# Performance work log

Measured on AMD Instinct MI355X. Metric: run time of the kernel, lower is better.

## Reference

```python
import jax, jax.numpy as jnp
import numpy as np

B, S = 1, 2048            # one prefill sequence, flattened to n_tokens = B*S
HID = 4096
NH, NKV, HD = 32, 8, 128  # query heads, kv heads, head dim
G, M = NKV, NH // NKV     # kv groups, query heads per group
THETA = 1e6


def setup_inputs() -> dict:
    key = jax.random.key(0)
    ks = jax.random.split(key, 5)
    h = jax.random.normal(ks[0], (B * S, HID), dtype=jnp.float32)
    position_ids = jnp.tile(jnp.arange(S, dtype=jnp.int32), B)
    wq = jax.random.normal(ks[1], (NH * HD, HID), dtype=jnp.float32) * 0.02
    wk = jax.random.normal(ks[2], (NKV * HD, HID), dtype=jnp.float32) * 0.02
    wv = jax.random.normal(ks[3], (NKV * HD, HID), dtype=jnp.float32) * 0.02
    wo = jax.random.normal(ks[4], (HID, NH * HD), dtype=jnp.float32) * 0.02
    return {"h": h, "position_ids": position_ids, "wq": wq, "wk": wk, "wv": wv, "wo": wo}


def _rope_cos_sin(position_ids):
    # non-interleaved (half-split) RoPE, default inv_freq with theta=1e6
    inv_freq = 1.0 / (THETA ** (jnp.arange(0, HD, 2, dtype=jnp.float32) / HD))  # [HD/2]
    freqs = position_ids.astype(jnp.float32)[:, None] * inv_freq[None, :]       # [n, HD/2]
    return jnp.cos(freqs)[:, None, :], jnp.sin(freqs)[:, None, :]               # broadcast over heads


def _apply_rope(x, cos, sin):
    x1, x2 = jnp.split(x, 2, axis=-1)
    return jnp.concatenate([x1 * cos - x2 * sin, x2 * cos + x1 * sin], axis=-1)


def reference(h, position_ids, wq, wk, wv, wo):
    n = h.shape[0]
    q = (h @ wq.T).reshape(n, NH, HD)
    k = (h @ wk.T).reshape(n, NKV, HD)
    v = (h @ wv.T).reshape(B, S, NKV, HD)

    cos, sin = _rope_cos_sin(position_ids)
    q = _apply_rope(q, cos, sin).reshape(B, S, G, M, HD)
    k = _apply_rope(k, cos, sin).reshape(B, S, G, HD)

    scale = 1.0 / np.sqrt(HD).astype(np.float32)
    # grouped-query attention: each kv head g serves M query heads
    scores = jnp.einsum('bqgmd,bkgd->bgmqk', q, k) * scale      # [B,G,M,S,S]
    causal = jnp.tril(jnp.ones((S, S), dtype=bool))
    scores = jnp.where(causal, scores, jnp.finfo(scores.dtype).min)
    p = jax.nn.softmax(scores, axis=-1)
    o = jnp.einsum('bgmqk,bkgd->bqgmd', p, v).reshape(n, NH * HD)
    return o @ wo.T
```

## Files before the change

kernel.cpp:

```cpp
#include <hip/hip_runtime.h>
#include <hip/hip_bf16.h>

#define S_LEN 2048
#define HID 4096
#define NH 32
#define NKV 8
#define HD 128
#define NQKV 6144

typedef unsigned short u16;
typedef unsigned int u32;
typedef __bf16 bf16x8 __attribute__((ext_vector_type(8)));
typedef float f32x4 __attribute__((ext_vector_type(4)));

__device__ __forceinline__ float bf2f(u16 u) {
    union { u32 i; float f; } x; x.i = ((u32)u) << 16; return x.f;
}
__device__ __forceinline__ u16 f2bf(float f) {
    union { float f; u32 i; } x; x.f = f;
    u32 r = x.i + 0x7fffu + ((x.i >> 16) & 1u);
    return (u16)(r >> 16);
}
__device__ __forceinline__ u32 pack2(float a, float b) {
    return (u32)f2bf(a) | ((u32)f2bf(b) << 16);
}
__device__ __forceinline__ void gld16(const u16* g, u16* l) {
    __builtin_amdgcn_global_load_lds(
        (const __attribute__((address_space(1))) u32*)g,
        (__attribute__((address_space(3))) u32*)l, 16, 0, 0);
}

__global__ __launch_bounds__(256) void cvt_f32_bf16(
    const float* __restrict__ src, u16* __restrict__ dst, int n8)
{
    int i = blockIdx.x * 256 + threadIdx.x;
    if (i >= n8) return;
    const float4* s = (const float4*)src + (size_t)i * 2;
    float4 x0 = s[0], x1 = s[1];
    uint4 p;
    p.x = pack2(x0.x, x0.y); p.y = pack2(x0.z, x0.w);
    p.z = pack2(x1.x, x1.y); p.w = pack2(x1.z, x1.w);
    *((uint4*)dst + i) = p;
}

template <bool OUTBF16>
__global__ __launch_bounds__(256) void gemm128(
    const u16* __restrict__ X, const u16* __restrict__ W,
    void* __restrict__ C, int K, int ldc)
{
    __shared__ __align__(16) u16 As[128 * 32];
    __shared__ __align__(16) u16 Bs[128 * 32];

    const int tid  = threadIdx.x;
    const int w    = tid >> 6;
    const int lane = tid & 63;
    const int quad = lane >> 4;
    const int n16  = lane & 15;

    int id = blockIdx.y * gridDim.x + blockIdx.x;
    const int nwg = gridDim.x * gridDim.y;
    if ((nwg & 7) == 0) {
        const int cpx = nwg >> 3;
        id = (id & 7) * cpx + (id >> 3);
    }
    const int m0 = (id / gridDim.x) * 128;
    const int n0 = (id % gridDim.x) * 128;

    const int wr   = (w >> 1) * 64;
    const int wc   = (w & 1) * 64;

    const int c0 = tid;
    const int c1 = tid + 256;

    f32x4 acc[4][4] = {};

    for (int k0 = 0; k0 < K; k0 += 32) {
        __syncthreads();
        gld16(X + (size_t)(m0 + (c0 >> 2)) * K + k0 + (c0 & 3) * 8,
              As + (size_t)(w * 64) * 8);
        gld16(X + (size_t)(m0 + (c1 >> 2)) * K + k0 + (c1 & 3) * 8,
              As + (size_t)(256 + w * 64) * 8);
        gld16(W + (size_t)(n0 + (c0 >> 2)) * K + k0 + (c0 & 3) * 8,
              Bs + (size_t)(w * 64) * 8);
        gld16(W + (size_t)(n0 + (c1 >> 2)) * K + k0 + (c1 & 3) * 8,
              Bs + (size_t)(256 + w * 64) * 8);
        __syncthreads();

        bf16x8 a[4], b[4];
#pragma unroll
        for (int t = 0; t < 4; ++t) {
            a[t] = *reinterpret_cast<const bf16x8*>(As + (wr + t * 16 + n16) * 32 + quad * 8);
            b[t] = *reinterpret_cast<const bf16x8*>(Bs + (wc + t * 16 + n16) * 32 + quad * 8);
        }
#pragma unroll
        for (int mt = 0; mt < 4; ++mt)
#pragma unroll
            for (int nt = 0; nt < 4; ++nt)
                acc[mt][nt] = __builtin_amdgcn_mfma_f32_16x16x32_bf16(
                    a[mt], b[nt], acc[mt][nt], 0, 0, 0);
    }

#pragma unroll
    for (int mt = 0; mt < 4; ++mt) {
        const int row0 = m0 + wr + mt * 16 + quad * 4;
#pragma unroll
        for (int nt = 0; nt < 4; ++nt) {
            const int col = n0 + wc + nt * 16 + n16;
#pragma unroll
            for (int r = 0; r < 4; ++r) {
                if constexpr (OUTBF16)
                    ((u16*)C)[(size_t)(row0 + r) * ldc + col] = f2bf(acc[mt][nt][r]);
                else
                    ((float*)C)[(size_t)(row0 + r) * ldc + col] = acc[mt][nt][r];
            }
        }
    }
}

template <bool XF32, bool OUTBF16>
__global__ __launch_bounds__(256) void gemm_bt(
    const void* __restrict__ Xv,
    const float* __restrict__ W0, int r1,
    const float* __restrict__ W1, int r2,
    const float* __restrict__ W2,
    void* __restrict__ C, int K, int ldc)
{
    __shared__ u16 Xs[64][48];
    __shared__ u16 Ws[64][48];

    const int tid  = threadIdx.x;
    const int w    = tid >> 6;
    const int lane = tid & 63;
    const int m0   = blockIdx.y * 64;
    const int n0   = blockIdx.x * 64;

    const int sr = tid >> 2;
    const int sc = (tid & 3) * 8;

    const float* xrow32 = nullptr;
    const u16*   xrow16 = nullptr;
    if constexpr (XF32) xrow32 = (const float*)Xv + (size_t)(m0 + sr) * K;
    else                xrow16 = (const u16*)Xv + (size_t)(m0 + sr) * K;

    const int wr = n0 + sr;
    const float* wrow;
    if (wr < r1)      wrow = W0 + (size_t)wr * K;
    else if (wr < r2) wrow = W1 + (size_t)(wr - r1) * K;
    else              wrow = W2 + (size_t)(wr - r2) * K;

    f32x4 acc[4] = {};
    const int mrow = w * 16 + (lane & 15);
    const int nrow = lane & 15;
    const int kq   = (lane >> 4) * 8;

    for (int k0 = 0; k0 < K; k0 += 32) {
        __syncthreads();
        if constexpr (XF32) {
            float4 x0 = *reinterpret_cast<const float4*>(xrow32 + k0 + sc);
            float4 x1 = *reinterpret_cast<const float4*>(xrow32 + k0 + sc + 4);
            uint4 p;
            p.x = pack2(x0.x, x0.y); p.y = pack2(x0.z, x0.w);
            p.z = pack2(x1.x, x1.y); p.w = pack2(x1.z, x1.w);
            *reinterpret_cast<uint4*>(&Xs[sr][sc]) = p;
        } else {
            *reinterpret_cast<uint4*>(&Xs[sr][sc]) =
                *reinterpret_cast<const uint4*>(xrow16 + k0 + sc);
        }
        {
            float4 w0v = *reinterpret_cast<const float4*>(wrow + k0 + sc);
            float4 w1v = *reinterpret_cast<const float4*>(wrow + k0 + sc + 4);
            uint4 p;
            p.x = pack2(w0v.x, w0v.y); p.y = pack2(w0v.z, w0v.w);
            p.z = pack2(w1v.x, w1v.y); p.w = pack2(w1v.z, w1v.w);
            *reinterpret_cast<uint4*>(&Ws[sr][sc]) = p;
        }
        __syncthreads();
        bf16x8 a = *reinterpret_cast<const bf16x8*>(&Xs[mrow][kq]);
#pragma unroll
        for (int t = 0; t < 4; ++t) {
            bf16x8 b = *reinterpret_cast<const bf16x8*>(&Ws[t * 16 + nrow][kq]);
            acc[t] = __builtin_amdgcn_mfma_f32_16x16x32_bf16(a, b, acc[t], 0, 0, 0);
        }
    }

    const int mb = m0 + w * 16 + ((lane >> 4) << 2);
#pragma unroll
    for (int t = 0; t < 4; ++t) {
        const int col = n0 + t * 16 + (lane & 15);
#pragma unroll
        for (int i = 0; i < 4; ++i) {
            if constexpr (OUTBF16)
                ((u16*)C)[(size_t)(mb + i) * ldc + col] = f2bf(acc[t][i]);
            else
                ((float*)C)[(size_t)(mb + i) * ldc + col] = acc[t][i];
        }
    }
}

__global__ __launch_bounds__(256) void rope_kernel(
    const u16* __restrict__ qkv, const int* __restrict__ pos,
    u16* __restrict__ qb, u16* __restrict__ kb, u16* __restrict__ vb)
{
    const int n   = blockIdx.x;
    const int tid = threadIdx.x;
    const float scale = 0.08838834764831845f;
    __shared__ float cs[64], sn[64];
    if (tid < 64) {
        float p   = (float)pos[n];
        float inv = powf(1.0e6f, -(float)tid / 64.0f);
        float f   = p * inv;
        cs[tid] = cosf(f);
        sn[tid] = sinf(f);
    }
    __syncthreads();
    const u16* row = qkv + (size_t)n * NQKV;

    for (int i = tid; i < NH * 64; i += 256) {
        int h = i >> 6, j = i & 63;
        float x1 = bf2f(row[h * HD + j]), x2 = bf2f(row[h * HD + j + 64]);
        size_t base = ((size_t)h * S_LEN + n) * HD;
        qb[base + j]      = f2bf((x1 * cs[j] - x2 * sn[j]) * scale);
        qb[base + j + 64] = f2bf((x2 * cs[j] + x1 * sn[j]) * scale);
    }
    for (int i = tid; i < NKV * 64; i += 256) {
        int g = i >> 6, j = i & 63;
        const u16* kr = row + NH * HD + g * HD;
        float x1 = bf2f(kr[j]), x2 = bf2f(kr[j + 64]);
        size_t base = ((size_t)g * S_LEN + n) * HD;
        kb[base + j]      = f2bf(x1 * cs[j] - x2 * sn[j]);
        kb[base + j + 64] = f2bf(x2 * cs[j] + x1 * sn[j]);
    }
    for (int i = tid; i < NKV * HD; i += 256) {
        int g = i >> 7, d = i & 127;
        vb[((size_t)g * S_LEN + n) * HD + d] = row[NH * HD + NKV * HD + g * HD + d];
    }
}

__global__ __launch_bounds__(256) void attn_mfma(
    const u16* __restrict__ qb, const u16* __restrict__ kb,
    const u16* __restrict__ vb, u16* __restrict__ ao)
{
    __shared__ __align__(16) u16 KPs[64 * 128];
    __shared__ __align__(16) u16 Vt[128 * 64];

    const int tid  = threadIdx.x;
    const int w    = tid >> 6;
    const int lane = tid & 63;
    const int quad = lane >> 4;
    const int n16  = lane & 15;
    const int h    = blockIdx.y;
    const int g    = h >> 2;
    const int NQT  = S_LEN / 64;

    const u16* kbase = kb + (size_t)g * S_LEN * HD;
    const u16* vbase = vb + (size_t)g * S_LEN * HD;
    const int xsw = (n16 & 7) << 3;

    for (int half = 0; half < 2; ++half) {
        const int qt = half ? (NQT - 1 - blockIdx.x) : blockIdx.x;
        const int q0 = qt * 64;

        bf16x8 qf[4];
        {
            const u16* qrow = qb + ((size_t)h * S_LEN + q0 + w * 16 + n16) * HD;
#pragma unroll
            for (int s = 0; s < 4; ++s)
                qf[s] = *reinterpret_cast<const bf16x8*>(qrow + s * 32 + quad * 8);
        }

        f32x4 of[8] = {};
        float mrow[4], lrow[4];
#pragma unroll
        for (int r = 0; r < 4; ++r) { mrow[r] = -1e30f; lrow[r] = 0.0f; }

        uint4 kreg[4], vreg[4];
        auto load_kv = [&](int k0) {
#pragma unroll
            for (int i = 0; i < 4; ++i) {
                kreg[i] = *reinterpret_cast<const uint4*>(
                    kbase + (size_t)(k0 + (tid >> 4) + 16 * i) * HD + (tid & 15) * 8);
                vreg[i] = *reinterpret_cast<const uint4*>(
                    vbase + (size_t)(k0 + lane) * HD + w * 8 + i * 32);
            }
        };
        load_kv(0);

        const int ntiles = qt + 1;
        for (int kt = 0; kt < ntiles; ++kt) {
            __syncthreads();
#pragma unroll
            for (int i = 0; i < 4; ++i) {
                const int key = (tid >> 4) + 16 * i;
                const int d0  = (tid & 15) * 8;
                *reinterpret_cast<uint4*>(
                    &KPs[key * 128 + (d0 ^ ((key & 7) << 3))]) = kreg[i];
            }
#pragma unroll
            for (int i = 0; i < 4; ++i) {
                const int d0 = w * 8 + i * 32;
                const u32 vw[4] = {vreg[i].x, vreg[i].y, vreg[i].z, vreg[i].w};
#pragma unroll
                for (int t = 0; t < 4; ++t) {
                    const int r0 = d0 + 2 * t;
                    Vt[r0 * 64 + (lane ^ ((r0 & 7) << 3))]             = (u16)(vw[t] & 0xffff);
                    Vt[(r0 + 1) * 64 + (lane ^ (((r0 + 1) & 7) << 3))] = (u16)(vw[t] >> 16);
                }
            }
            __syncthreads();
            if (kt + 1 < ntiles) load_kv((kt + 1) * 64);

            f32x4 sc[4] = {};
#pragma unroll
            for (int s = 0; s < 4; ++s) {
#pragma unroll
                for (int t = 0; t < 4; ++t) {
                    bf16x8 bf = *reinterpret_cast<const bf16x8*>(
                        &KPs[(t * 16 + n16) * 128 + ((s * 32 + quad * 8) ^ xsw)]);
                    sc[t] = __builtin_amdgcn_mfma_f32_16x16x32_bf16(qf[s], bf, sc[t], 0, 0, 0);
                }
            }

            if (kt == ntiles - 1) {
                const int qbase = q0 + w * 16 + quad * 4;
#pragma unroll
                for (int t = 0; t < 4; ++t) {
                    int key = kt * 64 + t * 16 + n16;
#pragma unroll
                    for (int r = 0; r < 4; ++r)
                        if (key > qbase + r) sc[t][r] = -1e30f;
                }
            }

            __syncthreads();

#pragma unroll
            for (int r = 0; r < 4; ++r) {
                float mx = fmaxf(fmaxf(sc[0][r], sc[1][r]), fmaxf(sc[2][r], sc[3][r]));
                mx = fmaxf(mx, __shfl_xor(mx, 1));
                mx = fmaxf(mx, __shfl_xor(mx, 2));
                mx = fmaxf(mx, __shfl_xor(mx, 4));
                mx = fmaxf(mx, __shfl_xor(mx, 8));
                float mnew  = fmaxf(mrow[r], mx);
                float alpha = __expf(mrow[r] - mnew);
                float ls = 0.0f;
                const int pr = quad * 4 + r;
#pragma unroll
                for (int t = 0; t < 4; ++t) {
                    float p = __expf(sc[t][r] - mnew);
                    KPs[(w * 16 + pr) * 64 + ((t * 16 + n16) ^ ((pr & 7) << 3))] = f2bf(p);
                    ls += p;
                }
                ls += __shfl_xor(ls, 1);
                ls += __shfl_xor(ls, 2);
                ls += __shfl_xor(ls, 4);
                ls += __shfl_xor(ls, 8);
                lrow[r] = lrow[r] * alpha + ls;
                mrow[r] = mnew;
#pragma unroll
                for (int nt = 0; nt < 8; ++nt) of[nt][r] *= alpha;
            }
            __threadfence_block();

#pragma unroll
            for (int s = 0; s < 2; ++s) {
                bf16x8 af = *reinterpret_cast<const bf16x8*>(
                    &KPs[(w * 16 + n16) * 64 + ((s * 32 + quad * 8) ^ xsw)]);
#pragma unroll
                for (int nt = 0; nt < 8; ++nt) {
                    bf16x8 bf = *reinterpret_cast<const bf16x8*>(
                        &Vt[(nt * 16 + n16) * 64 + ((s * 32 + quad * 8) ^ xsw)]);
                    of[nt] = __builtin_amdgcn_mfma_f32_16x16x32_bf16(af, bf, of[nt], 0, 0, 0);
                }
            }
        }

#pragma unroll
        for (int r = 0; r < 4; ++r) {
            float inv = 1.0f / lrow[r];
            u16* dst = ao + (size_t)(q0 + w * 16 + quad * 4 + r) * (NH * HD) + h * HD + n16;
#pragma unroll
            for (int nt = 0; nt < 8; ++nt)
                dst[nt * 16] = f2bf(of[nt][r] * inv);
        }
    }
}

extern "C" void kernel_launch(void* const* d_in, const int* in_sizes, int n_in,
                              void* d_out, int out_size, void* d_ws, size_t ws_size,
                              hipStream_t stream)
{
    const float* h   = (const float*)d_in[0];
    const int*   pos = (const int*)d_in[1];
    const float* wq  = (const float*)d_in[2];
    const float* wk  = (const float*)d_in[3];
    const float* wv  = (const float*)d_in[4];
    const float* wo  = (const float*)d_in[5];

    char* ws = (char*)d_ws;

    if (ws_size >= 92274688ull) {
        u16* hb     = (u16*)(ws);
        u16* wqkv_b = (u16*)(ws + 16777216);
        u16* ao     = (u16*)(ws + 16777216);
        u16* kb     = (u16*)(ws + 33554432);
        u16* vb     = (u16*)(ws + 37748736);
        u16* wo_b   = (u16*)(ws + 41943040);
        u16* qkv    = (u16*)(ws + 67108864);
        u16* qb     = hb;

        cvt_f32_bf16<<<4096, 256, 0, stream>>>(h, hb, 1048576);
        cvt_f32_bf16<<<8192, 256, 0, stream>>>(wq, wqkv_b, 2097152);
        cvt_f32_bf16<<<2048, 256, 0, stream>>>(wk, wqkv_b + 16777216, 524288);
        cvt_f32_bf16<<<2048, 256, 0, stream>>>(wv, wqkv_b + 20971520, 524288);

        gemm128<true><<<dim3(NQKV / 128, S_LEN / 128), 256, 0, stream>>>(
            hb, wqkv_b, qkv, HID, NQKV);
        rope_kernel<<<S_LEN, 256, 0, stream>>>(qkv, pos, qb, kb, vb);
        cvt_f32_bf16<<<8192, 256, 0, stream>>>(wo, wo_b, 2097152);
        attn_mfma<<<dim3(S_LEN / 128, NH), 256, 0, stream>>>(qb, kb, vb, ao);
        gemm128<false><<<dim3(HID / 128, S_LEN / 128), 256, 0, stream>>>(
            ao, wo_b, d_out, NH * HD, HID);
    } else {
        u16* qkv = (u16*)(ws);
        u16* qb  = (u16*)(ws + 25165824);
        u16* kb  = (u16*)(ws + 41943040);
        u16* vb  = (u16*)(ws + 46137344);
        u16* ao  = (u16*)(ws + 50331648);

        dim3 g1(NQKV / 64, S_LEN / 64);
        gemm_bt<true, true><<<g1, 256, 0, stream>>>(
            h, wq, NH * HD, wk, NH * HD + NKV * HD, wv, qkv, HID, NQKV);
        rope_kernel<<<S_LEN, 256, 0, stream>>>(qkv, pos, qb, kb, vb);
        attn_mfma<<<dim3(S_LEN / 128, NH), 256, 0, stream>>>(qb, kb, vb, ao);
        dim3 g2(HID / 64, S_LEN / 64);
        gemm_bt<false, false><<<g2, 256, 0, stream>>>(
            ao, wo, HID, wo, HID, wo, d_out, NH * HD, HID);
    }
}
```

Before: 581.4 us.

## Split attention key range across two thread groups with split-K softmax merge

Doubles the attention block to 512 threads, with two 256-thread groups each processing alternating key tiles using separate K/P and V^T shared-memory buffers. At the end the partial outputs, row maxes and row sums are merged through shared memory using log-sum-exp rescaling. This is meant to raise parallelism and latency hiding in the attention kernel, which had only 512 blocks of 4 waves. In exchange it doubles shared memory per block to 64 KB, adds extra barriers and a merge step, and leaves one group idle on odd tile counts.

```diff
diff --git a/kernel.cpp b/kernel.cpp
--- a/kernel.cpp
+++ b/kernel.cpp
@@ -236,15 +236,16 @@
     }
 }
 
-__global__ __launch_bounds__(256) void attn_mfma(
+__global__ __launch_bounds__(512, 4) void attn_mfma(
     const u16* __restrict__ qb, const u16* __restrict__ kb,
     const u16* __restrict__ vb, u16* __restrict__ ao)
 {
-    __shared__ __align__(16) u16 KPs[64 * 128];
-    __shared__ __align__(16) u16 Vt[128 * 64];
+    __shared__ __align__(16) u16 smem[32768];
 
     const int tid  = threadIdx.x;
-    const int w    = tid >> 6;
+    const int gtid = tid & 255;
+    const int grp  = tid >> 8;
+    const int wg   = (tid >> 6) & 3;
     const int lane = tid & 63;
     const int quad = lane >> 4;
     const int n16  = lane & 15;
@@ -252,6 +253,10 @@
     const int g    = h >> 2;
     const int NQT  = S_LEN / 64;
 
+    u16* KPg = smem + grp * 8192;
+    u16* Vtg = smem + 16384 + grp * 8192;
+    float* mb = reinterpret_cast<float*>(smem);
+
     const u16* kbase = kb + (size_t)g * S_LEN * HD;
     const u16* vbase = vb + (size_t)g * S_LEN * HD;
     const int xsw = (n16 & 7) << 3;
@@ -262,7 +267,7 @@
 
         bf16x8 qf[4];
         {
-            const u16* qrow = qb + ((size_t)h * S_LEN + q0 + w * 16 + n16) * HD;
+            const u16* qrow = qb + ((size_t)h * S_LEN + q0 + wg * 16 + n16) * HD;
 #pragma unroll
             for (int s = 0; s < 4; ++s)
                 qf[s] = *reinterpret_cast<const bf16x8*>(qrow + s * 32 + quad * 8);
@@ -278,110 +283,138 @@
 #pragma unroll
             for (int i = 0; i < 4; ++i) {
                 kreg[i] = *reinterpret_cast<const uint4*>(
-                    kbase + (size_t)(k0 + (tid >> 4) + 16 * i) * HD + (tid & 15) * 8);
+                    kbase + (size_t)(k0 + (gtid >> 4) + 16 * i) * HD + (gtid & 15) * 8);
                 vreg[i] = *reinterpret_cast<const uint4*>(
-                    vbase + (size_t)(k0 + lane) * HD + w * 8 + i * 32);
+                    vbase + (size_t)(k0 + lane) * HD + wg * 8 + i * 32);
             }
         };
-        load_kv(0);
+        load_kv(grp * 64);
 
         const int ntiles = qt + 1;
-        for (int kt = 0; kt < ntiles; ++kt) {
+        const int nIt = (ntiles + 1) >> 1;
+        for (int it = 0; it < nIt; ++it) {
+            const int kt = 2 * it + grp;
+            const bool act = (kt < ntiles);
+
             __syncthreads();
-#pragma unroll
-            for (int i = 0; i < 4; ++i) {
-                const int key = (tid >> 4) + 16 * i;
-                const int d0  = (tid & 15) * 8;
-                *reinterpret_cast<uint4*>(
-                    &KPs[key * 128 + (d0 ^ ((key & 7) << 3))]) = kreg[i];
-            }
-#pragma unroll
-            for (int i = 0; i < 4; ++i) {
-                const int d0 = w * 8 + i * 32;
-                const u32 vw[4] = {vreg[i].x, vreg[i].y, vreg[i].z, vreg[i].w};
-#pragma unroll
-                for (int t = 0; t < 4; ++t) {
-                    const int r0 = d0 + 2 * t;
-                    Vt[r0 * 64 + (lane ^ ((r0 & 7) << 3))]             = (u16)(vw[t] & 0xffff);
-                    Vt[(r0 + 1) * 64 + (lane ^ (((r0 + 1) & 7) << 3))] = (u16)(vw[t] >> 16);
+            if (act) {
+#pragma unroll
+                for (int i = 0; i < 4; ++i) {
+                    const int key = (gtid >> 4) + 16 * i;
+                    const int d0  = (gtid & 15) * 8;
+                    *reinterpret_cast<uint4*>(
+                        &KPg[key * 128 + (d0 ^ ((key & 7) << 3))]) = kreg[i];
+                }
+#pragma unroll
+                for (int i = 0; i < 4; ++i) {
+                    const int d0 = wg * 8 + i * 32;
+                    const u32 vw[4] = {vreg[i].x, vreg[i].y, vreg[i].z, vreg[i].w};
+#pragma unroll
+                    for (int t = 0; t < 4; ++t) {
+                        const int r0 = d0 + 2 * t;
+                        Vtg[r0 * 64 + (lane ^ ((r0 & 7) << 3))]             = (u16)(vw[t] & 0xffff);
+                        Vtg[(r0 + 1) * 64 + (lane ^ (((r0 + 1) & 7) << 3))] = (u16)(vw[t] >> 16);
+                    }
                 }
             }
             __syncthreads();
-            if (kt + 1 < ntiles) load_kv((kt + 1) * 64);
+            if (kt + 2 < ntiles) load_kv((kt + 2) * 64);
 
             f32x4 sc[4] = {};
-#pragma unroll
-            for (int s = 0; s < 4; ++s) {
-#pragma unroll
-                for (int t = 0; t < 4; ++t) {
-                    bf16x8 bf = *reinterpret_cast<const bf16x8*>(
-                        &KPs[(t * 16 + n16) * 128 + ((s * 32 + quad * 8) ^ xsw)]);
-                    sc[t] = __builtin_amdgcn_mfma_f32_16x16x32_bf16(qf[s], bf, sc[t], 0, 0, 0);
-                }
-            }
-
-            if (kt == ntiles - 1) {
-                const int qbase = q0 + w * 16 + quad * 4;
-#pragma unroll
-                for (int t = 0; t < 4; ++t) {
-                    int key = kt * 64 + t * 16 + n16;
-#pragma unroll
-                    for (int r = 0; r < 4; ++r)
-                        if (key > qbase + r) sc[t][r] = -1e30f;
+            if (act) {
+#pragma unroll
+                for (int s = 0; s < 4; ++s) {
+#pragma unroll
+                    for (int t = 0; t < 4; ++t) {
+                        bf16x8 bf = *reinterpret_cast<const bf16x8*>(
+                            &KPg[(t * 16 + n16) * 128 + ((s * 32 + quad * 8) ^ xsw)]);
+                        sc[t] = __builtin_amdgcn_mfma_f32_16x16x32_bf16(qf[s], bf, sc[t], 0, 0, 0);
+                    }
+                }
+                if (kt == qt) {
+                    const int qbase = q0 + wg * 16 + quad * 4;
+#pragma unroll
+                    for (int t = 0; t < 4; ++t) {
+                        int key = kt * 64 + t * 16 + n16;
+#pragma unroll
+                        for (int r = 0; r < 4; ++r)
+                            if (key > qbase + r) sc[t][r] = -1e30f;
+                    }
                 }
             }
 
             __syncthreads();
 
+            if (act) {
+#pragma unroll
+                for (int r = 0; r < 4; ++r) {
+                    float mx = fmaxf(fmaxf(sc[0][r], sc[1][r]), fmaxf(sc[2][r], sc[3][r]));
+                    mx = fmaxf(mx, __shfl_xor(mx, 1));
+                    mx = fmaxf(mx, __shfl_xor(mx, 2));
+                    mx = fmaxf(mx, __shfl_xor(mx, 4));
+                    mx = fmaxf(mx, __shfl_xor(mx, 8));
+                    float mnew  = fmaxf(mrow[r], mx);
+                    float alpha = __expf(mrow[r] - mnew);
+                    float ls = 0.0f;
+                    const int pr = quad * 4 + r;
+#pragma unroll
+                    for (int t = 0; t < 4; ++t) {
+                        float p = __expf(sc[t][r] - mnew);
+                        KPg[(wg * 16 + pr) * 64 + ((t * 16 + n16) ^ ((pr & 7) << 3))] = f2bf(p);
+                        ls += p;
+                    }
+                    ls += __shfl_xor(ls, 1);
+                    ls += __shfl_xor(ls, 2);
+                    ls += __shfl_xor(ls, 4);
+                    ls += __shfl_xor(ls, 8);
+                    lrow[r] = lrow[r] * alpha + ls;
+                    mrow[r] = mnew;
+#pragma unroll
+                    for (int nt = 0; nt < 8; ++nt) of[nt][r] *= alpha;
+                }
+                __threadfence_block();
+
+#pragma unroll
+                for (int s = 0; s < 2; ++s) {
+                    bf16x8 af = *reinterpret_cast<const bf16x8*>(
+                        &KPg[(wg * 16 + n16) * 64 + ((s * 32 + quad * 8) ^ xsw)]);
+#pragma unroll
+                    for (int nt = 0; nt < 8; ++nt) {
+                        bf16x8 bf = *reinterpret_cast<const bf16x8*>(
+                            &Vtg[(nt * 16 + n16) * 64 + ((s * 32 + quad * 8) ^ xsw)]);
+                        of[nt] = __builtin_amdgcn_mfma_f32_16x16x32_bf16(af, bf, of[nt], 0, 0, 0);
+                    }
+                }
+            }
+        }
+
+        __syncthreads();
+        if (grp == 1) {
+            float* dst = mb + ((size_t)(wg * 64 + lane)) * 40;
+#pragma unroll
+            for (int nt = 0; nt < 8; ++nt)
+#pragma unroll
+                for (int r = 0; r < 4; ++r) dst[nt * 4 + r] = of[nt][r];
+#pragma unroll
+            for (int r = 0; r < 4; ++r) { dst[32 + r] = mrow[r]; dst[36 + r] = lrow[r]; }
+        }
+        __syncthreads();
+        if (grp == 0) {
+            const float* src = mb + ((size_t)(wg * 64 + lane)) * 40;
 #pragma unroll
             for (int r = 0; r < 4; ++r) {
-                float mx = fmaxf(fmaxf(sc[0][r], sc[1][r]), fmaxf(sc[2][r], sc[3][r]));
-                mx = fmaxf(mx, __shfl_xor(mx, 1));
-                mx = fmaxf(mx, __shfl_xor(mx, 2));
-                mx = fmaxf(mx, __shfl_xor(mx, 4));
-                mx = fmaxf(mx, __shfl_xor(mx, 8));
-                float mnew  = fmaxf(mrow[r], mx);
-                float alpha = __expf(mrow[r] - mnew);
-                float ls = 0.0f;
-                const int pr = quad * 4 + r;
-#pragma unroll
-                for (int t = 0; t < 4; ++t) {
-                    float p = __expf(sc[t][r] - mnew);
-                    KPs[(w * 16 + pr) * 64 + ((t * 16 + n16) ^ ((pr & 7) << 3))] = f2bf(p);
-                    ls += p;
-                }
-                ls += __shfl_xor(ls, 1);
-                ls += __shfl_xor(ls, 2);
-                ls += __shfl_xor(ls, 4);
-                ls += __shfl_xor(ls, 8);
-                lrow[r] = lrow[r] * alpha + ls;
-                mrow[r] = mnew;
-#pragma unroll
-                for (int nt = 0; nt < 8; ++nt) of[nt][r] *= alpha;
-            }
-            __threadfence_block();
-
-#pragma unroll
-            for (int s = 0; s < 2; ++s) {
-                bf16x8 af = *reinterpret_cast<const bf16x8*>(
-                    &KPs[(w * 16 + n16) * 64 + ((s * 32 + quad * 8) ^ xsw)]);
-#pragma unroll
-                for (int nt = 0; nt < 8; ++nt) {
-                    bf16x8 bf = *reinterpret_cast<const bf16x8*>(
-                        &Vt[(nt * 16 + n16) * 64 + ((s * 32 + quad * 8) ^ xsw)]);
-                    of[nt] = __builtin_amdgcn_mfma_f32_16x16x32_bf16(af, bf, of[nt], 0, 0, 0);
-                }
-            }
-        }
-
-#pragma unroll
-        for (int r = 0; r < 4; ++r) {
-            float inv = 1.0f / lrow[r];
-            u16* dst = ao + (size_t)(q0 + w * 16 + quad * 4 + r) * (NH * HD) + h * HD + n16;
-#pragma unroll
-            for (int nt = 0; nt < 8; ++nt)
-                dst[nt * 16] = f2bf(of[nt][r] * inv);
-        }
+                const float mB = src[32 + r], lB = src[36 + r];
+                const float m  = fmaxf(mrow[r], mB);
+                const float a  = __expf(mrow[r] - m);
+                const float b  = __expf(mB - m);
+                const float inv = 1.0f / (lrow[r] * a + lB * b);
+                u16* dst = ao + (size_t)(q0 + wg * 16 + quad * 4 + r) * (NH * HD) + h * HD + n16;
+#pragma unroll
+                for (int nt = 0; nt < 8; ++nt)
+                    dst[nt * 16] = f2bf((of[nt][r] * a + src[nt * 4 + r] * b) * inv);
+            }
+        }
+        __syncthreads();
     }
 }
 
@@ -417,7 +450,7 @@
             hb, wqkv_b, qkv, HID, NQKV);
         rope_kernel<<<S_LEN, 256, 0, stream>>>(qkv, pos, qb, kb, vb);
         cvt_f32_bf16<<<8192, 256, 0, stream>>>(wo, wo_b, 2097152);
-        attn_mfma<<<dim3(S_LEN / 128, NH), 256, 0, stream>>>(qb, kb, vb, ao);
+        attn_mfma<<<dim3(S_LEN / 128, NH), 512, 0, stream>>>(qb, kb, vb, ao);
         gemm128<false><<<dim3(HID / 128, S_LEN / 128), 256, 0, stream>>>(
             ao, wo_b, d_out, NH * HD, HID);
     } else {
@@ -431,7 +464,7 @@
         gemm_bt<true, true><<<g1, 256, 0, stream>>>(
             h, wq, NH * HD, wk, NH * HD + NKV * HD, wv, qkv, HID, NQKV);
         rope_kernel<<<S_LEN, 256, 0, stream>>>(qkv, pos, qb, kb, vb);
-        attn_mfma<<<dim3(S_LEN / 128, NH), 256, 0, stream>>>(qb, kb, vb, ao);
+        attn_mfma<<<dim3(S_LEN / 128, NH), 512, 0, stream>>>(qb, kb, vb, ao);
         dim3 g2(HID / 64, S_LEN / 64);
         gemm_bt<false, false><<<g2, 256, 0, stream>>>(
             ao, wo, HID, wo, HID, wo, d_out, NH * HD, HID);
```

Result: slower. 699.5 us (+20.3%).
